# Optimization experiments

Measured on AMD Instinct MI355X. Metric: run time of the kernel, lower is better.

Reference implementation:

```python
import jax, jax.numpy as jnp
import numpy as np

N = 50000
E = 800000
IN_C = 128
OUT_C = 128
EPS = 1e-5


def _w(key, i, o, scale=0.02):
    return jax.random.normal(key, (i, o), dtype=jnp.float32) * scale


def setup_inputs() -> dict:
    key = jax.random.key(0)
    ks = jax.random.split(key, 20)
    x = jax.random.normal(ks[0], (N, IN_C), dtype=jnp.float32)
    edge_index = jax.random.randint(ks[1], (2, E), 0, N, dtype=jnp.int64)
    C = OUT_C
    return {
        "x": x,
        "edge_index": edge_index,
        # conv1: SAGEConv(IN_C -> 2C): lin_l (neighbors, with bias), lin_r (root, no bias)
        "Wl1": _w(ks[2], IN_C, 2 * C), "bl1": jnp.zeros((2 * C,), jnp.float32),
        "Wr1": _w(ks[3], IN_C, 2 * C),
        "ln1_w": jnp.ones((2 * C,), jnp.float32), "ln1_b": jnp.zeros((2 * C,), jnp.float32),
        "W1": _w(ks[4], 2 * C, 4 * C), "b1": jnp.zeros((4 * C,), jnp.float32),
        "W2": _w(ks[5], 4 * C, 2 * C), "b2": jnp.zeros((2 * C,), jnp.float32),
        # conv2: SAGEConv(2C -> C)
        "Wl2": _w(ks[6], 2 * C, C), "bl2": jnp.zeros((C,), jnp.float32),
        "Wr2": _w(ks[7], 2 * C, C),
        "ln2_w": jnp.ones((C,), jnp.float32), "ln2_b": jnp.zeros((C,), jnp.float32),
        "W3": _w(ks[8], C, 2 * C), "b3": jnp.zeros((2 * C,), jnp.float32),
        "W4": _w(ks[9], 2 * C, C), "b4": jnp.zeros((C,), jnp.float32),
    }


def _sage_conv(x, src, dst, Wl, bl, Wr):
    # mean aggregation of source features at destination nodes
    n = x.shape[0]
    msg = x[src]                                              # [E, F]
    agg = jax.ops.segment_sum(msg, dst, num_segments=n)       # [N, F]
    deg = jax.ops.segment_sum(jnp.ones((src.shape[0], 1), x.dtype), dst, num_segments=n)
    agg = agg / jnp.maximum(deg, 1.0)                         # empty neighborhoods -> 0
    return agg @ Wl + bl + x @ Wr


def _graph_layernorm(x, w, b):
    # PyG LayerNorm mode='graph' (single graph): normalize over all nodes and features
    mu = x.mean()
    xc = x - mu
    var = (xc * xc).mean()
    return xc * jax.lax.rsqrt(var + EPS) * w + b


def reference(x, edge_index, Wl1, bl1, Wr1, ln1_w, ln1_b, W1, b1, W2, b2,
              Wl2, bl2, Wr2, ln2_w, ln2_b, W3, b3, W4, b4):
    src, dst = edge_index[0], edge_index[1]
    h = _sage_conv(x, src, dst, Wl1, bl1, Wr1)
    h = jax.nn.relu(_graph_layernorm(h, ln1_w, ln1_b))
    h = jax.nn.relu(h @ W1 + b1)
    h = jax.nn.relu(h @ W2 + b2)
    h = _sage_conv(h, src, dst, Wl2, bl2, Wr2)
    h = jax.nn.relu(_graph_layernorm(h, ln2_w, ln2_b))
    h = jax.nn.relu(h @ W3 + b3)
    return h @ W4 + b4
```

## Files before the change

kernel.cpp:

```cpp
#include <hip/hip_runtime.h>

#define NN   50000
#define EE   800000
#define MPAD 50048
#define NBLK ((NN + 255) / 256)

typedef __bf16 bf16x8 __attribute__((ext_vector_type(8)));
typedef float  vfloat4 __attribute__((ext_vector_type(4)));
typedef short  vshort4 __attribute__((ext_vector_type(4)));
typedef short  vshort8 __attribute__((ext_vector_type(8)));

__device__ __forceinline__ short f2bf(float f) {
  union { float f; unsigned u; } v; v.f = f;
  unsigned r = v.u + 0x7FFFu + ((v.u >> 16) & 1u);
  return (short)(r >> 16);
}
__device__ __forceinline__ float bf2f(short h) {
  union { unsigned u; float f; } v; v.u = ((unsigned)(unsigned short)h) << 16;
  return v.f;
}

__device__ __forceinline__ void load_lds16(const short* g, short* l) {
  __builtin_amdgcn_global_load_lds(
      (__attribute__((address_space(1))) void*)(void*)g,
      (__attribute__((address_space(3))) void*)(void*)l, 16, 0, 0);
}

__global__ __launch_bounds__(256) void detect_kernel(const unsigned* __restrict__ e,
                                                     int* __restrict__ flag) {
  unsigned v = 0;
  for (int i = threadIdx.x; i < 2048; i += 256) v |= e[2 * i + 1];
  for (int o = 32; o; o >>= 1) v |= (unsigned)__shfl_down((int)v, o, 64);
  __shared__ unsigned r[4];
  if ((threadIdx.x & 63) == 0) r[threadIdx.x >> 6] = v;
  __syncthreads();
  if (threadIdx.x == 0) flag[0] = ((r[0] | r[1] | r[2] | r[3]) == 0) ? 1 : 0;
}

__global__ __launch_bounds__(256) void degree_kernel(const void* __restrict__ edges,
                                                     const int* __restrict__ flag,
                                                     int* __restrict__ deg) {
  int e = blockIdx.x * 256 + threadIdx.x;
  if (e >= EE) return;
  int d = flag[0] ? (int)((const long long*)edges)[EE + e] : ((const int*)edges)[EE + e];
  atomicAdd(&deg[d], 1);
}

__global__ __launch_bounds__(256) void scan_local(const int* __restrict__ deg,
                                                  int* __restrict__ iscan,
                                                  int* __restrict__ bsum) {
  __shared__ int tmp[256];
  int t = threadIdx.x;
  int i = blockIdx.x * 256 + t;
  int v = (i < NN) ? deg[i] : 0;
  tmp[t] = v;
  __syncthreads();
  int acc = v;
  for (int d = 1; d < 256; d <<= 1) {
    int u = (t >= d) ? tmp[t - d] : 0;
    __syncthreads();
    acc += u;
    tmp[t] = acc;
    __syncthreads();
  }
  if (i < NN) iscan[i] = acc - v;
  if (t == 255) bsum[blockIdx.x] = acc;
}

__global__ __launch_bounds__(256) void scan_apply(const int* __restrict__ iscan,
                                                  const int* __restrict__ bsum,
                                                  int* __restrict__ offs,
                                                  int* __restrict__ cursor) {
  __shared__ int sh[256];
  int t = threadIdx.x;
  int v = (t < NBLK) ? bsum[t] : 0;
  sh[t] = (t < (int)blockIdx.x) ? v : 0;
  __syncthreads();
  for (int d = 128; d; d >>= 1) { if (t < d) sh[t] += sh[t + d]; __syncthreads(); }
  int base = sh[0];
  __syncthreads();
  sh[t] = v;
  __syncthreads();
  for (int d = 128; d; d >>= 1) { if (t < d) sh[t] += sh[t + d]; __syncthreads(); }
  int total = sh[0];
  int i = blockIdx.x * 256 + t;
  if (i < NN) { int off = iscan[i] + base; offs[i] = off; cursor[i] = off; }
  if (blockIdx.x == gridDim.x - 1 && t == 0) offs[NN] = total;
}

__global__ __launch_bounds__(256) void fill_kernel(const void* __restrict__ edges,
                                                   const int* __restrict__ flag,
                                                   int* __restrict__ cursor,
                                                   int* __restrict__ csr) {
  int e = blockIdx.x * 256 + threadIdx.x;
  if (e >= EE) return;
  int sv, dv;
  if (flag[0]) {
    sv = (int)((const long long*)edges)[e];
    dv = (int)((const long long*)edges)[EE + e];
  } else {
    sv = ((const int*)edges)[e];
    dv = ((const int*)edges)[EE + e];
  }
  int p = atomicAdd(&cursor[dv], 1);
  __builtin_nontemporal_store(sv, &csr[p]);
}

__global__ __launch_bounds__(256) void xcast_kernel(const float* __restrict__ x,
                                                    short* __restrict__ xbf) {
  int i = blockIdx.x * 256 + threadIdx.x;
  if (i >= NN * 128 / 8) return;
  vfloat4 v0 = *(const vfloat4*)(x + (size_t)i * 8);
  vfloat4 v1 = *(const vfloat4*)(x + (size_t)i * 8 + 4);
  vshort8 o;
  o[0] = f2bf(v0.x); o[1] = f2bf(v0.y); o[2] = f2bf(v0.z); o[3] = f2bf(v0.w);
  o[4] = f2bf(v1.x); o[5] = f2bf(v1.y); o[6] = f2bf(v1.z); o[7] = f2bf(v1.w);
  *(vshort8*)(xbf + (size_t)i * 8) = o;
}

__global__ __launch_bounds__(256) void prep_all(
    const float* __restrict__ Wl1, const float* __restrict__ Wr1,
    const float* __restrict__ W1,  const float* __restrict__ W2,
    const float* __restrict__ Wl2, const float* __restrict__ Wr2,
    const float* __restrict__ W3,  const float* __restrict__ W4,
    short* __restrict__ wc1T, short* __restrict__ w1T, short* __restrict__ w2T,
    short* __restrict__ wlr2T, short* __restrict__ w3T, short* __restrict__ w4T) {
  int b = blockIdx.x;
  if (b >= 1280 && b < 1536) {
    int idx = (b - 1280) * 256 + threadIdx.x;
    int n = idx >> 8, k = idx & 255;
    float v = (n < 128) ? Wl2[(size_t)k * 128 + n] : Wr2[(size_t)k * 128 + (n - 128)];
    wlr2T[idx] = f2bf(v);
    return;
  }
  const float *s0, *s1; short* dst; int K0, logK, Nc, base;
  if      (b <  256) { s0=Wl1; s1=Wr1; dst=wc1T; K0=128; logK=8; Nc=256; base=0;    }
  else if (b <  768) { s0=W1;  s1=W1;  dst=w1T;  K0=256; logK=8; Nc=512; base=256;  }
  else if (b < 1280) { s0=W2;  s1=W2;  dst=w2T;  K0=512; logK=9; Nc=256; base=768;  }
  else if (b < 1664) { s0=W3;  s1=W3;  dst=w3T;  K0=128; logK=7; Nc=256; base=1536; }
  else               { s0=W4;  s1=W4;  dst=w4T;  K0=256; logK=8; Nc=128; base=1664; }
  int idx = (b - base) * 256 + threadIdx.x;
  int n = idx >> logK, k = idx & ((1 << logK) - 1);
  float v = (k < K0) ? s0[(size_t)k * Nc + n] : s1[(size_t)(k - K0) * Nc + n];
  dst[idx] = f2bf(v);
}

__global__ __launch_bounds__(256) void prep_bias(const float* __restrict__ bl2,
                                                 float* __restrict__ cbias) {
  int t = threadIdx.x;
  cbias[t] = (t < 128) ? 0.f : bl2[t - 128];
}

__global__ __launch_bounds__(256) void reduce_stats(const float* __restrict__ part,
                                                    int n, float* __restrict__ out) {
  float s = 0.f, s2 = 0.f;
  for (int i = threadIdx.x; i < n; i += 256) { s += part[2 * i]; s2 += part[2 * i + 1]; }
  for (int o = 32; o; o >>= 1) {
    s  += __shfl_down(s,  o, 64);
    s2 += __shfl_down(s2, o, 64);
  }
  __shared__ float ps[8];
  int lane = threadIdx.x & 63, wv = threadIdx.x >> 6;
  if (lane == 0) { ps[wv] = s; ps[wv + 4] = s2; }
  __syncthreads();
  if (threadIdx.x == 0) {
    out[0] = ps[0] + ps[1] + ps[2] + ps[3];
    out[1] = ps[4] + ps[5] + ps[6] + ps[7];
  }
}

template<int CONCAT>
__global__ __launch_bounds__(256) void agg_mean(const short* __restrict__ src,
                                                const int* __restrict__ offs,
                                                const int* __restrict__ csr,
                                                short* __restrict__ dst) {
  int node = blockIdx.x * 4 + (threadIdx.x >> 6);
  int lane = threadIdx.x & 63;
  if (node >= MPAD) return;
  short* row = dst + (size_t)node * (CONCAT ? 256 : 128);
  if (node >= NN) {
    if (CONCAT) *(vshort4*)(row + lane * 4) = (vshort4){0, 0, 0, 0};
    else if (lane < 32) *(vshort4*)(row + lane * 4) = (vshort4){0, 0, 0, 0};
    return;
  }
  int g = lane >> 4, sub = lane & 15;
  int e0 = offs[node], e1 = offs[node + 1];
  float a0[8] = {0, 0, 0, 0, 0, 0, 0, 0};
  float a1[8] = {0, 0, 0, 0, 0, 0, 0, 0};
  int e = e0;
  while (e < e1) {
    int cnt = e1 - e; if (cnt > 64) cnt = 64;
    int myidx = (lane < cnt) ? csr[e + lane] : 0;
    for (int i = 0; i < cnt; i += 8) {
      int p0 = g + i;
      int p1 = g + i + 4;
      int s0 = __shfl(myidx, p0, 64);
      int s1 = __shfl(myidx, p1, 64);
      if (p0 < cnt) {
        vshort8 v0 = *(const vshort8*)(src + (size_t)s0 * 128 + sub * 8);
#pragma unroll
        for (int j = 0; j < 8; j++) a0[j] += bf2f(v0[j]);
      }
      if (p1 < cnt) {
        vshort8 v1 = *(const vshort8*)(src + (size_t)s1 * 128 + sub * 8);
#pragma unroll
        for (int j = 0; j < 8; j++) a1[j] += bf2f(v1[j]);
      }
    }
    e += cnt;
  }
#pragma unroll
  for (int j = 0; j < 8; j++) {
    a0[j] += a1[j];
    a0[j] += __shfl_down(a0[j], 32, 64);
    a0[j] += __shfl_down(a0[j], 16, 64);
  }
  float inv = (e1 > e0) ? 1.f / (float)(e1 - e0) : 0.f;
  if (g == 0) {
    vshort8 o;
#pragma unroll
    for (int j = 0; j < 8; j++) o[j] = f2bf(a0[j] * inv);
    *(vshort8*)(row + sub * 8) = o;
  } else if (CONCAT && g == 1) {
    *(vshort8*)(row + 128 + sub * 8) = *(const vshort8*)(src + (size_t)node * 128 + sub * 8);
  }
}

__global__ __launch_bounds__(256) void add_stats(const short* __restrict__ r2,
                                                 const short* __restrict__ a2,
                                                 short* __restrict__ h_d,
                                                 float* __restrict__ partials) {
  int i = blockIdx.x * 256 + threadIdx.x;
  const int tot8 = MPAD * 128 / 8, real8 = NN * 128 / 8;
  float s = 0.f, s2 = 0.f;
  if (i < tot8) {
    if (i >= real8) {
      *(vshort8*)(h_d + (size_t)i * 8) = (vshort8){0,0,0,0,0,0,0,0};
    } else {
      vshort8 rv = *(const vshort8*)(r2 + (size_t)i * 8);
      vshort8 av = *(const vshort8*)(a2 + (size_t)i * 8);
      vshort8 o;
#pragma unroll
      for (int j = 0; j < 8; j++) {
        float v = bf2f(rv[j]) + bf2f(av[j]);
        s += v; s2 += v * v;
        o[j] = f2bf(v);
      }
      *(vshort8*)(h_d + (size_t)i * 8) = o;
    }
  }
  int lane = threadIdx.x & 63, wave = threadIdx.x >> 6;
  for (int o2 = 32; o2; o2 >>= 1) {
    s  += __shfl_down(s,  o2, 64);
    s2 += __shfl_down(s2, o2, 64);
  }
  __shared__ float ps[8];
  if (lane == 0) { ps[wave] = s; ps[wave + 4] = s2; }
  __syncthreads();
  if (threadIdx.x == 0) {
    partials[2 * blockIdx.x]     = ps[0] + ps[1] + ps[2] + ps[3];
    partials[2 * blockIdx.x + 1] = ps[4] + ps[5] + ps[6] + ps[7];
  }
}

__global__ __launch_bounds__(256) void ln_apply(const short* __restrict__ h,
                                                const float* __restrict__ stats,
                                                const float* __restrict__ w,
                                                const float* __restrict__ b,
                                                short* __restrict__ out,
                                                int realElems, int totElems, int F,
                                                float invCount) {
  int base = (blockIdx.x * blockDim.x + threadIdx.x) * 4;
  if (base >= totElems) return;
  if (base >= realElems) { *(vshort4*)(out + base) = (vshort4){0,0,0,0}; return; }
  float mu  = stats[0] * invCount;
  float var = stats[1] * invCount - mu * mu;
  float rs  = rsqrtf(var + 1e-5f);
  int col = base % F;
  vshort4 hv = *(const vshort4*)(h + base);
  vshort4 o;
  o.x = f2bf(fmaxf((bf2f(hv.x) - mu) * rs * w[col]     + b[col],     0.f));
  o.y = f2bf(fmaxf((bf2f(hv.y) - mu) * rs * w[col + 1] + b[col + 1], 0.f));
  o.z = f2bf(fmaxf((bf2f(hv.z) - mu) * rs * w[col + 2] + b[col + 2], 0.f));
  o.w = f2bf(fmaxf((bf2f(hv.w) - mu) * rs * w[col + 3] + b[col + 3], 0.f));
  *(vshort4*)(out + base) = o;
}

template<int RELU, int OUTBF, int BOUND, int STATS, int SPLIT>
__global__ __launch_bounds__(256) void gemm_bt(const short* __restrict__ A,
                                               const short* __restrict__ BT,
                                               const float* __restrict__ bias,
                                               float* __restrict__ Cf,
                                               short* __restrict__ Cb,
                                               short* __restrict__ Cb2,
                                               float* __restrict__ partials,
                                               int Nc, int K, int Mreal) {
  __shared__ short lsA[128 * 64];
  __shared__ short lsB[128 * 64];
  const int tid  = threadIdx.x;
  const int lane = tid & 63;
  const int wave = tid >> 6;
  const int wr   = (wave >> 1) << 6;
  const int wc   = (wave & 1) << 6;
  const int row0 = blockIdx.y << 7;
  const int col0 = blockIdx.x << 7;
  const int r16  = lane & 15;
  const int quad = lane >> 4;
  const int srow   = lane >> 3;
  const int schunk = lane & 7;
  const int sxoff  = ((schunk ^ srow) << 3);

  vfloat4 acc[4][4];
#pragma unroll
  for (int i = 0; i < 4; i++)
#pragma unroll
    for (int j = 0; j < 4; j++) acc[i][j] = (vfloat4){0.f, 0.f, 0.f, 0.f};

  for (int k0 = 0; k0 < K; k0 += 64) {
    __syncthreads();
#pragma unroll
    for (int t = 0; t < 4; t++) {
      int seg  = (wave << 2) + t;
      int trow = (seg << 3) + srow;
      load_lds16(A  + (size_t)(row0 + trow) * K + k0 + sxoff, lsA + (seg << 9) + lane * 8);
      load_lds16(BT + (size_t)(col0 + trow) * K + k0 + sxoff, lsB + (seg << 9) + lane * 8);
    }
    __syncthreads();
#pragma unroll
    for (int kk = 0; kk < 64; kk += 32) {
      int kf8 = (kk >> 3) + quad;
      bf16x8 af[4], bfr[4];
#pragma unroll
      for (int i = 0; i < 4; i++) {
        int r = wr + (i << 4) + r16;
        af[i] = *(const bf16x8*)(lsA + (r << 6) + ((kf8 ^ (r & 7)) << 3));
      }
#pragma unroll
      for (int j = 0; j < 4; j++) {
        int r = wc + (j << 4) + r16;
        bfr[j] = *(const bf16x8*)(lsB + (r << 6) + ((kf8 ^ (r & 7)) << 3));
      }
#pragma unroll
      for (int i = 0; i < 4; i++)
#pragma unroll
        for (int j = 0; j < 4; j++)
          acc[i][j] = __builtin_amdgcn_mfma_f32_16x16x32_bf16(bfr[j], af[i], acc[i][j], 0, 0, 0);
    }
  }

  float s = 0.f, s2 = 0.f;
#pragma unroll
  for (int i = 0; i < 4; i++) {
    int gr = row0 + wr + (i << 4) + r16;
    if (BOUND && gr >= Mreal) continue;
#pragma unroll
    for (int j = 0; j < 4; j++) {
      int gc = col0 + wc + (j << 4) + (quad << 2);
      vfloat4 bv = *(const vfloat4*)(bias + gc);
      vfloat4 v;
#pragma unroll
      for (int p = 0; p < 4; p++) {
        float t = acc[i][j][p] + bv[p];
        if (STATS) { s += t; s2 += t * t; }
        if (RELU) t = fmaxf(t, 0.f);
        v[p] = t;
      }
      if (OUTBF) {
        vshort4 o;
#pragma unroll
        for (int p = 0; p < 4; p++) o[p] = f2bf(v[p]);
        if (SPLIT) {
          if (gc < 128) *(vshort4*)(Cb  + (size_t)gr * 128 + gc)       = o;
          else          *(vshort4*)(Cb2 + (size_t)gr * 128 + gc - 128) = o;
        } else {
          *(vshort4*)(Cb + (size_t)gr * Nc + gc) = o;
        }
      } else {
        *(vfloat4*)(Cf + (size_t)gr * Nc + gc) = v;
      }
    }
  }
  if (STATS) {
    for (int o2 = 32; o2; o2 >>= 1) {
      s  += __shfl_down(s,  o2, 64);
      s2 += __shfl_down(s2, o2, 64);
    }
    __shared__ float ps[8];
    if (lane == 0) { ps[wave] = s; ps[wave + 4] = s2; }
    __syncthreads();
    if (tid == 0) {
      int bid = blockIdx.y * gridDim.x + blockIdx.x;
      partials[2 * bid]     = ps[0] + ps[1] + ps[2] + ps[3];
      partials[2 * bid + 1] = ps[4] + ps[5] + ps[6] + ps[7];
    }
  }
}

extern "C" void kernel_launch(void* const* d_in, const int* in_sizes, int n_in,
                              void* d_out, int out_size, void* d_ws, size_t ws_size,
                              hipStream_t stream) {
  const float* x    = (const float*)d_in[0];
  const void*  edge = d_in[1];
  const float* Wl1  = (const float*)d_in[2];
  const float* bl1  = (const float*)d_in[3];
  const float* Wr1  = (const float*)d_in[4];
  const float* ln1w = (const float*)d_in[5];
  const float* ln1b = (const float*)d_in[6];
  const float* W1   = (const float*)d_in[7];
  const float* b1   = (const float*)d_in[8];
  const float* W2   = (const float*)d_in[9];
  const float* b2   = (const float*)d_in[10];
  const float* Wl2  = (const float*)d_in[11];
  const float* bl2  = (const float*)d_in[12];
  const float* Wr2  = (const float*)d_in[13];
  const float* ln2w = (const float*)d_in[14];
  const float* ln2b = (const float*)d_in[15];
  const float* W3   = (const float*)d_in[16];
  const float* b3   = (const float*)d_in[17];
  const float* W4   = (const float*)d_in[18];
  const float* b4   = (const float*)d_in[19];
  float* out = (float*)d_out;

  char* wsp = (char*)d_ws;
  size_t o = 0;
  auto alloc = [&](size_t bytes) -> void* {
    void* p = wsp + o;
    o = (o + bytes + 255) & ~(size_t)255;
    return p;
  };
  int*   flag   = (int*)alloc(4);
  int*   deg    = (int*)alloc((size_t)NN * 4);
  int*   iscan  = (int*)alloc((size_t)NN * 4);
  int*   bsum   = (int*)alloc((size_t)NBLK * 4);
  int*   offs   = (int*)alloc((size_t)(NN + 1) * 4);
  int*   cursor = (int*)alloc((size_t)NN * 4);
  int*   csr    = (int*)alloc((size_t)EE * 4);
  float* stats  = (float*)alloc(32);
  float* cbias  = (float*)alloc(256 * 4);
  float* pb1    = (float*)alloc(782 * 2 * 4);
  float* pb2    = (float*)alloc(3128 * 2 * 4);
  short* wc1T   = (short*)alloc(256 * 256 * 2);
  short* w1T    = (short*)alloc(512 * 256 * 2);
  short* w2T    = (short*)alloc(256 * 512 * 2);
  short* wlr2T  = (short*)alloc(256 * 256 * 2);
  short* w3T    = (short*)alloc(256 * 128 * 2);
  short* w4T    = (short*)alloc(128 * 256 * 2);
  char*  bufB   = (char*)alloc((size_t)MPAD * 512);
  char*  bufA   = (char*)alloc((size_t)MPAD * 1024);

  const size_t Q = (size_t)MPAD * 256;
  short* xbf = (short*)bufA;
  short* h1  = (short*)bufA;
  short* h_b = (short*)bufA;
  short* p2  = (short*)bufA;
  short* r2  = (short*)(bufA + Q);
  short* a2  = (short*)(bufA + 2 * Q);
  short* h_d = (short*)(bufA + 3 * Q);
  short* h_e = (short*)bufA;
  short* h_f = (short*)(bufA + Q);
  short* hcat1 = (short*)bufB;
  short* h_a   = (short*)bufB;
  short* h_c   = (short*)bufB;

  hipMemsetAsync(deg, 0, (size_t)NN * 4, stream);
  detect_kernel<<<1, 256, 0, stream>>>((const unsigned*)edge, flag);
  degree_kernel<<<(EE + 255) / 256, 256, 0, stream>>>(edge, flag, deg);
  scan_local<<<NBLK, 256, 0, stream>>>(deg, iscan, bsum);
  scan_apply<<<NBLK, 256, 0, stream>>>(iscan, bsum, offs, cursor);
  fill_kernel<<<(EE + 255) / 256, 256, 0, stream>>>(edge, flag, cursor, csr);

  xcast_kernel<<<(NN * 128 / 8 + 255) / 256, 256, 0, stream>>>(x, xbf);
  prep_all<<<1792, 256, 0, stream>>>(Wl1, Wr1, W1, W2, Wl2, Wr2, W3, W4,
                                     wc1T, w1T, w2T, wlr2T, w3T, w4T);
  prep_bias<<<1, 256, 0, stream>>>(bl2, cbias);

  agg_mean<1><<<MPAD / 4, 256, 0, stream>>>(xbf, offs, csr, hcat1);
  gemm_bt<0, 1, 1, 1, 0><<<dim3(2, MPAD / 128), 256, 0, stream>>>(
      hcat1, wc1T, bl1, nullptr, h1, nullptr, pb1, 256, 256, NN);
  reduce_stats<<<1, 256, 0, stream>>>(pb1, 782, stats);
  ln_apply<<<(MPAD * 256 / 4 + 255) / 256, 256, 0, stream>>>(
      h1, stats, ln1w, ln1b, h_a, NN * 256, MPAD * 256, 256, 1.f / (NN * 256.f));
  gemm_bt<1, 1, 0, 0, 0><<<dim3(4, MPAD / 128), 256, 0, stream>>>(
      h_a, w1T, b1, nullptr, h_b, nullptr, nullptr, 512, 256, MPAD);
  gemm_bt<1, 1, 0, 0, 0><<<dim3(2, MPAD / 128), 256, 0, stream>>>(
      h_b, w2T, b2, nullptr, h_c, nullptr, nullptr, 256, 512, MPAD);

  gemm_bt<0, 1, 0, 0, 1><<<dim3(2, MPAD / 128), 256, 0, stream>>>(
      h_c, wlr2T, cbias, nullptr, p2, r2, nullptr, 256, 256, MPAD);
  agg_mean<0><<<MPAD / 4, 256, 0, stream>>>(p2, offs, csr, a2);
  add_stats<<<MPAD * 128 / 8 / 256, 256, 0, stream>>>(r2, a2, h_d, pb2);
  reduce_stats<<<1, 256, 0, stream>>>(pb2, 3128, stats + 2);
  ln_apply<<<(MPAD * 128 / 4 + 255) / 256, 256, 0, stream>>>(
      h_d, stats + 2, ln2w, ln2b, h_e, NN * 128, MPAD * 128, 128, 1.f / (NN * 128.f));
  gemm_bt<1, 1, 0, 0, 0><<<dim3(2, MPAD / 128), 256, 0, stream>>>(
      h_e, w3T, b3, nullptr, h_f, nullptr, nullptr, 256, 128, MPAD);
  gemm_bt<0, 0, 1, 0, 0><<<dim3(1, MPAD / 128), 256, 0, stream>>>(
      h_f, w4T, b4, out, nullptr, nullptr, nullptr, 128, 256, NN);
}
```

Before: 463.4 us.

## Build CSR via two-level bucket sort with shared-memory atomics

Replaces the global-atomic degree count, two-pass scan, and atomic scatter fill with a two-level binning scheme. Edges are first bucketed by destination into 196 buckets of 256 nodes using LDS histograms and staged as packed (src,dst) pairs. Each bucket is then sorted locally in shared memory to produce offsets and CSR entries. The aim is to cut the cost of random global atomics and to improve locality of the CSR writes, at the price of an extra staging buffer and additional passes over the edge list.

```diff
diff --git a/kernel.cpp b/kernel.cpp
--- a/kernel.cpp
+++ b/kernel.cpp
@@ -3,7 +3,7 @@
 #define NN   50000
 #define EE   800000
 #define MPAD 50048
-#define NBLK ((NN + 255) / 256)
+#define NBUCK 196
 
 typedef __bf16 bf16x8 __attribute__((ext_vector_type(8)));
 typedef float  vfloat4 __attribute__((ext_vector_type(4)));
@@ -37,22 +37,33 @@
   if (threadIdx.x == 0) flag[0] = ((r[0] | r[1] | r[2] | r[3]) == 0) ? 1 : 0;
 }
 
-__global__ __launch_bounds__(256) void degree_kernel(const void* __restrict__ edges,
-                                                     const int* __restrict__ flag,
-                                                     int* __restrict__ deg) {
-  int e = blockIdx.x * 256 + threadIdx.x;
-  if (e >= EE) return;
-  int d = flag[0] ? (int)((const long long*)edges)[EE + e] : ((const int*)edges)[EE + e];
-  atomicAdd(&deg[d], 1);
-}
-
-__global__ __launch_bounds__(256) void scan_local(const int* __restrict__ deg,
-                                                  int* __restrict__ iscan,
-                                                  int* __restrict__ bsum) {
+
+__global__ __launch_bounds__(256) void bin_count(const void* __restrict__ edges,
+                                                 const int* __restrict__ flag,
+                                                 int* __restrict__ bcnt) {
+  __shared__ int h[NBUCK];
+  int t = threadIdx.x;
+  for (int i = t; i < NBUCK; i += 256) h[i] = 0;
+  __syncthreads();
+  const int per = (EE + NBUCK - 1) / NBUCK;
+  int lo = blockIdx.x * per, hi = lo + per;
+  if (hi > EE) hi = EE;
+  int fl = flag[0];
+  for (int e = lo + t; e < hi; e += 256) {
+    int dv = fl ? (int)((const long long*)edges)[EE + e] : ((const int*)edges)[EE + e];
+    atomicAdd(&h[dv >> 8], 1);
+  }
+  __syncthreads();
+  for (int i = t; i < NBUCK; i += 256)
+    if (h[i]) atomicAdd(&bcnt[i], h[i]);
+}
+
+__global__ __launch_bounds__(256) void bin_scan(const int* __restrict__ bcnt,
+                                                int* __restrict__ bstart,
+                                                int* __restrict__ bcur) {
   __shared__ int tmp[256];
   int t = threadIdx.x;
-  int i = blockIdx.x * 256 + t;
-  int v = (i < NN) ? deg[i] : 0;
+  int v = (t < NBUCK) ? bcnt[t] : 0;
   tmp[t] = v;
   __syncthreads();
   int acc = v;
@@ -63,47 +74,82 @@
     tmp[t] = acc;
     __syncthreads();
   }
-  if (i < NN) iscan[i] = acc - v;
-  if (t == 255) bsum[blockIdx.x] = acc;
-}
-
-__global__ __launch_bounds__(256) void scan_apply(const int* __restrict__ iscan,
-                                                  const int* __restrict__ bsum,
+  int excl = acc - v;
+  if (t < NBUCK) { bstart[t] = excl; bcur[t] = excl; }
+  if (t == NBUCK - 1) bstart[NBUCK] = excl + v;
+}
+
+__global__ __launch_bounds__(256) void bin_scatter(const void* __restrict__ edges,
+                                                   const int* __restrict__ flag,
+                                                   int* __restrict__ bcur,
+                                                   long long* __restrict__ staging) {
+  __shared__ int h[NBUCK];
+  __shared__ int base[NBUCK];
+  int t = threadIdx.x;
+  for (int i = t; i < NBUCK; i += 256) h[i] = 0;
+  __syncthreads();
+  const int per = (EE + NBUCK - 1) / NBUCK;
+  int lo = blockIdx.x * per, hi = lo + per;
+  if (hi > EE) hi = EE;
+  int fl = flag[0];
+  for (int e = lo + t; e < hi; e += 256) {
+    int dv = fl ? (int)((const long long*)edges)[EE + e] : ((const int*)edges)[EE + e];
+    atomicAdd(&h[dv >> 8], 1);
+  }
+  __syncthreads();
+  for (int i = t; i < NBUCK; i += 256) {
+    int c = h[i];
+    base[i] = c ? atomicAdd(&bcur[i], c) : 0;
+    h[i] = 0;
+  }
+  __syncthreads();
+  for (int e = lo + t; e < hi; e += 256) {
+    int sv, dv;
+    if (fl) { sv = (int)((const long long*)edges)[e]; dv = (int)((const long long*)edges)[EE + e]; }
+    else    { sv = ((const int*)edges)[e];            dv = ((const int*)edges)[EE + e]; }
+    int b = dv >> 8;
+    int r = atomicAdd(&h[b], 1);
+    staging[base[b] + r] = ((long long)sv << 32) | (unsigned)dv;
+  }
+}
+
+__global__ __launch_bounds__(256) void bucket_csr(const int* __restrict__ bstart,
+                                                  const long long* __restrict__ staging,
                                                   int* __restrict__ offs,
-                                                  int* __restrict__ cursor) {
-  __shared__ int sh[256];
-  int t = threadIdx.x;
-  int v = (t < NBLK) ? bsum[t] : 0;
-  sh[t] = (t < (int)blockIdx.x) ? v : 0;
-  __syncthreads();
-  for (int d = 128; d; d >>= 1) { if (t < d) sh[t] += sh[t + d]; __syncthreads(); }
-  int base = sh[0];
-  __syncthreads();
-  sh[t] = v;
-  __syncthreads();
-  for (int d = 128; d; d >>= 1) { if (t < d) sh[t] += sh[t + d]; __syncthreads(); }
-  int total = sh[0];
-  int i = blockIdx.x * 256 + t;
-  if (i < NN) { int off = iscan[i] + base; offs[i] = off; cursor[i] = off; }
-  if (blockIdx.x == gridDim.x - 1 && t == 0) offs[NN] = total;
-}
-
-__global__ __launch_bounds__(256) void fill_kernel(const void* __restrict__ edges,
-                                                   const int* __restrict__ flag,
-                                                   int* __restrict__ cursor,
-                                                   int* __restrict__ csr) {
-  int e = blockIdx.x * 256 + threadIdx.x;
-  if (e >= EE) return;
-  int sv, dv;
-  if (flag[0]) {
-    sv = (int)((const long long*)edges)[e];
-    dv = (int)((const long long*)edges)[EE + e];
-  } else {
-    sv = ((const int*)edges)[e];
-    dv = ((const int*)edges)[EE + e];
-  }
-  int p = atomicAdd(&cursor[dv], 1);
-  __builtin_nontemporal_store(sv, &csr[p]);
+                                                  int* __restrict__ csr) {
+  int b = blockIdx.x, t = threadIdx.x;
+  int n0 = b << 8;
+  int s0 = bstart[b], s1 = bstart[b + 1];
+  __shared__ int cnt[256], tmp[256], cur[256];
+  cnt[t] = 0;
+  __syncthreads();
+  for (int i = s0 + t; i < s1; i += 256)
+    atomicAdd(&cnt[((int)(staging[i] & 0xffffffffLL)) - n0], 1);
+  __syncthreads();
+  int v = cnt[t];
+  tmp[t] = v;
+  __syncthreads();
+  int acc = v;
+  for (int d = 1; d < 256; d <<= 1) {
+    int u = (t >= d) ? tmp[t - d] : 0;
+    __syncthreads();
+    acc += u;
+    tmp[t] = acc;
+    __syncthreads();
+  }
+  int excl = acc - v;
+  int node = n0 + t;
+  if (node < NN) offs[node] = s0 + excl;
+  cur[t] = s0 + excl;
+  __syncthreads();
+  for (int i = s0 + t; i < s1; i += 256) {
+    long long pk = staging[i];
+    int dv = (int)(pk & 0xffffffffLL);
+    int sv = (int)(pk >> 32);
+    int p = atomicAdd(&cur[dv - n0], 1);
+    csr[p] = sv;
+  }
+  if (b == 0 && t == 0) offs[NN] = EE;
 }
 
 __global__ __launch_bounds__(256) void xcast_kernel(const float* __restrict__ x,
@@ -429,12 +475,12 @@
     return p;
   };
   int*   flag   = (int*)alloc(4);
-  int*   deg    = (int*)alloc((size_t)NN * 4);
-  int*   iscan  = (int*)alloc((size_t)NN * 4);
-  int*   bsum   = (int*)alloc((size_t)NBLK * 4);
+  int*   bcnt   = (int*)alloc(NBUCK * 4);
+  int*   bstart = (int*)alloc((NBUCK + 1) * 4);
+  int*   bcur   = (int*)alloc(NBUCK * 4);
   int*   offs   = (int*)alloc((size_t)(NN + 1) * 4);
-  int*   cursor = (int*)alloc((size_t)NN * 4);
   int*   csr    = (int*)alloc((size_t)EE * 4);
+  long long* staging = (long long*)alloc((size_t)EE * 8);
   float* stats  = (float*)alloc(32);
   float* cbias  = (float*)alloc(256 * 4);
   float* pb1    = (float*)alloc(782 * 2 * 4);
@@ -462,12 +508,12 @@
   short* h_a   = (short*)bufB;
   short* h_c   = (short*)bufB;
 
-  hipMemsetAsync(deg, 0, (size_t)NN * 4, stream);
+  hipMemsetAsync(bcnt, 0, NBUCK * 4, stream);
   detect_kernel<<<1, 256, 0, stream>>>((const unsigned*)edge, flag);
-  degree_kernel<<<(EE + 255) / 256, 256, 0, stream>>>(edge, flag, deg);
-  scan_local<<<NBLK, 256, 0, stream>>>(deg, iscan, bsum);
-  scan_apply<<<NBLK, 256, 0, stream>>>(iscan, bsum, offs, cursor);
-  fill_kernel<<<(EE + 255) / 256, 256, 0, stream>>>(edge, flag, cursor, csr);
+  bin_count<<<NBUCK, 256, 0, stream>>>(edge, flag, bcnt);
+  bin_scan<<<1, 256, 0, stream>>>(bcnt, bstart, bcur);
+  bin_scatter<<<NBUCK, 256, 0, stream>>>(edge, flag, bcur, staging);
+  bucket_csr<<<NBUCK, 256, 0, stream>>>(bstart, staging, offs, csr);
 
   xcast_kernel<<<(NN * 128 / 8 + 255) / 256, 256, 0, stream>>>(x, xbf);
   prep_all<<<1792, 256, 0, stream>>>(Wl1, Wr1, W1, W2, Wl2, Wr2, W3, W4,
```

Measured after the change: 403.0 us. 1.15x faster.
